# Kernel tuning notes

Hardware: AMD Instinct MI355X
Metric: run time of the kernel (lower is better)

## Reference

```python
import jax, jax.numpy as jnp
import numpy as np

K = 3        # kernel_size
DIL = 1      # dilation
PAD = 1      # padding (replicate)
RANKS = 3
STAGES = 9
C_OUT = 32


def setup_inputs() -> dict:
    key = jax.random.key(0)
    k1, k2, k3 = jax.random.split(key, 3)
    b, cin, H, W = 2, 3, 160, 160
    x = jax.random.normal(k1, (b, cin, H, W), dtype=jnp.float32)
    head_w = jax.random.normal(k2, (C_OUT, cin), dtype=jnp.float32) * (1.0 / np.sqrt(cin))
    tail_w = jax.random.normal(k3, (cin, C_OUT), dtype=jnp.float32) * (1.0 / np.sqrt(C_OUT))
    alphas = jnp.full((STAGES,), 0.01, dtype=jnp.float32)
    betas = jnp.full((STAGES,), 0.01, dtype=jnp.float32)
    return {"x": x, "head_w": head_w, "tail_w": tail_w, "alphas": alphas, "betas": betas}


def _unfold_like_torch(xp, H, W):
    # xp: [b, C, H+2p, W+2p] replicate-padded. Reproduce torch nn.Unfold output
    # layout [b, C*k*k, H*W] (channel-major, then ki, kj; L row-major over h,w).
    b, C = xp.shape[0], xp.shape[1]
    cols = [xp[:, :, i * DIL:i * DIL + H, j * DIL:j * DIL + W]
            for i in range(K) for j in range(K)]
    patches = jnp.stack(cols, axis=2)            # [b, C, k*k, H, W]
    return patches.reshape(b, C * K * K, H * W)  # torch unfold layout


def reference(x, head_w, tail_w, alphas, betas):
    b, cin, H, W = x.shape
    # head 1x1 conv (no bias) + relu
    xh = jax.nn.relu(jnp.einsum('bchw,oc->bohw', x, head_w))
    xp = jnp.pad(xh, ((0, 0), (0, 0), (PAD, PAD), (PAD, PAD)), mode='edge')
    Xu = _unfold_like_torch(xp, H, W)                 # [b, C*kk, H*W]
    # Faithful to torch: X = unfold.view(b, C, H, W, -1) (row-major reinterpret)
    X = Xu.reshape(b, C_OUT, H, W, K * K)
    U = jnp.repeat(X.mean(axis=-1, keepdims=True), RANKS, axis=-1)  # [b,C,H,W,r]
    V = jnp.repeat(X.mean(axis=1, keepdims=True), RANKS, axis=1)    # [b,r,H,W,kk]
    for i in range(STAGES):
        num_V = jnp.einsum('bchwr,bchwk->brhwk', U, X)
        UV = jnp.einsum('bchwr,brhwk->bchwk', U, V)
        den_V = jnp.einsum('bchwr,bchwk->brhwk', U, UV)
        V = V - betas[i] * (den_V - num_V)
        num_U = jnp.einsum('bchwk,brhwk->bchwr', X, V)
        UV = jnp.einsum('bchwr,brhwk->bchwk', U, V)
        den_U = jnp.einsum('bchwk,brhwk->bchwr', UV, V)
        U = U - alphas[i] * (den_U - num_U)
    center = (K // 2) * K + K // 2
    UVc = jnp.einsum('bchwr,brhwk->bchwk', U, V)[..., center]  # [b,C,H,W]
    out = jax.nn.relu(jnp.einsum('bchw,oc->bohw', UVc, tail_w))
    return out
```

## Files before the change

kernel.cpp:

```cpp
#include <hip/hip_runtime.h>
#include <hip/hip_bf16.h>

#define NB    2
#define HW    25600
#define WDIM  160
#define NSTG  9

template <int CTRL>
__device__ __forceinline__ float dpp_add(float v) {
    int moved = __builtin_amdgcn_update_dpp(0, __float_as_int(v), CTRL, 0xf, 0xf, true);
    return v + __int_as_float(moved);
}

__device__ __forceinline__ float reduce4(float v) {
    v = dpp_add<0xB1>(v);
    v = dpp_add<0x4E>(v);
    return v;
}

__global__ __launch_bounds__(256, 4) void fused_kernel(const float* __restrict__ x,
                                                       const float* __restrict__ head_w,
                                                       const float* __restrict__ tail_w,
                                                       const float* __restrict__ alphas,
                                                       const float* __restrict__ betas,
                                                       float* __restrict__ out) {
    int sub = threadIdx.x & 3;
    int pid = blockIdx.x * 64 + (threadIdx.x >> 2);
    int b   = blockIdx.x / 400;
    int s2  = pid - b * HW;
    int c0  = sub * 8;

    float al[NSTG], be[NSTG];
#pragma unroll
    for (int i = 0; i < NSTG; ++i) { al[i] = alphas[i]; be[i] = betas[i]; }

    const float* xb0 = x + b * 3 * HW;

    int g9  = s2 * 9;
    int kk0 = g9 / HW;
    int r0  = g9 - kk0 * HW;
    int h0  = r0 / WDIM;
    int w0  = r0 - h0 * WDIM;
    int ki0 = kk0 / 3;
    int dh0 = ki0 - 1,            dw0 = kk0 - ki0 * 3 - 1;
    int kk1 = kk0 + 1;
    int ki1 = kk1 / 3;
    int dh1 = ki1 - 1,            dw1 = kk1 - ki1 * 3 - 1;

    int p[9];
#pragma unroll
    for (int k2 = 0; k2 < 9; ++k2) {
        int r  = r0 + k2;
        int wn = w0 + k2;
        int cw = (wn >= WDIM);
        int w1 = cw ? wn - WDIM : wn;
        int h1 = h0 + cw;
        bool wr = (r >= HW);
        int h  = wr ? 0 : h1;
        int w  = wr ? r - HW : w1;
        int dh = wr ? dh1 : dh0;
        int dw = wr ? dw1 : dw0;
        int hh = min(max(h + dh, 0), 159);
        int ww = min(max(w + dw, 0), 159);
        p[k2]  = hh * WDIM + ww;
    }

    float xv0[9], xv1[9], xv2[9];
#pragma unroll
    for (int k2 = 0; k2 < 9; ++k2) xv0[k2] = xb0[p[k2]];
#pragma unroll
    for (int k2 = 0; k2 < 9; ++k2) xv1[k2] = xb0[HW + p[k2]];
#pragma unroll
    for (int k2 = 0; k2 < 9; ++k2) xv2[k2] = xb0[2 * HW + p[k2]];

    float X[9][8];
#pragma unroll
    for (int j = 0; j < 8; ++j) {
        float hwj0 = head_w[(c0 + j) * 3 + 0];
        float hwj1 = head_w[(c0 + j) * 3 + 1];
        float hwj2 = head_w[(c0 + j) * 3 + 2];
#pragma unroll
        for (int k2 = 0; k2 < 9; ++k2)
            X[k2][j] = fmaxf(hwj0 * xv0[k2] + hwj1 * xv1[k2] + hwj2 * xv2[k2], 0.f);
    }

    float u[8];
#pragma unroll
    for (int j = 0; j < 8; ++j) {
        float a = X[0][j];
#pragma unroll
        for (int k = 1; k < 9; ++k) a += X[k][j];
        u[j] = a * (1.f / 9.f);
    }
    float v[9];
#pragma unroll
    for (int k = 0; k < 9; ++k) {
        float pr = ((X[k][0] + X[k][1]) + (X[k][2] + X[k][3]))
                 + ((X[k][4] + X[k][5]) + (X[k][6] + X[k][7]));
        v[k] = reduce4(pr) * (1.f / 32.f);
    }

#pragma unroll
    for (int i = 0; i < NSTG; ++i) {
        float b3 = 3.f * be[i];
        float a3 = 3.f * al[i];
        float beta  = be[i];
        float alpha = al[i];
        float sp = ((u[0] * u[0] + u[1] * u[1]) + (u[2] * u[2] + u[3] * u[3]))
                 + ((u[4] * u[4] + u[5] * u[5]) + (u[6] * u[6] + u[7] * u[7]));
        float s  = reduce4(sp);
        float vs = 1.f - b3 * s;
#pragma unroll
        for (int k = 0; k < 9; ++k) {
            float qp = u[0] * X[k][0];
#pragma unroll
            for (int j = 1; j < 8; ++j) qp += u[j] * X[k][j];
            float q = reduce4(qp);
            v[k] = v[k] * vs + beta * q;
        }
        float t = (((v[0] * v[0] + v[1] * v[1]) + (v[2] * v[2] + v[3] * v[3]))
                +  ((v[4] * v[4] + v[5] * v[5]) + (v[6] * v[6] + v[7] * v[7])))
                +  v[8] * v[8];
        float us = 1.f - a3 * t;
#pragma unroll
        for (int j = 0; j < 8; ++j) {
            float m = X[0][j] * v[0];
#pragma unroll
            for (int k = 1; k < 9; ++k) m += X[k][j] * v[k];
            u[j] = u[j] * us + alpha * m;
        }
    }

    float v4 = v[4];
    float uvc[8];
#pragma unroll
    for (int j = 0; j < 8; ++j) uvc[j] = 3.f * u[j] * v4;
    float o[3];
#pragma unroll
    for (int oo = 0; oo < 3; ++oo) {
        const float* tw = tail_w + oo * 32 + c0;
        float pr = ((uvc[0] * tw[0] + uvc[1] * tw[1]) + (uvc[2] * tw[2] + uvc[3] * tw[3]))
                 + ((uvc[4] * tw[4] + uvc[5] * tw[5]) + (uvc[6] * tw[6] + uvc[7] * tw[7]));
        o[oo] = fmaxf(reduce4(pr), 0.f);
    }
    if (sub == 0) {
        float* op = out + b * 3 * HW + s2;
        op[0]      = o[0];
        op[HW]     = o[1];
        op[2 * HW] = o[2];
    }
}

extern "C" void kernel_launch(void* const* d_in, const int* in_sizes, int n_in,
                              void* d_out, int out_size, void* d_ws, size_t ws_size,
                              hipStream_t stream) {
    const float* x      = (const float*)d_in[0];
    const float* head_w = (const float*)d_in[1];
    const float* tail_w = (const float*)d_in[2];
    const float* alphas = (const float*)d_in[3];
    const float* betas  = (const float*)d_in[4];
    float*       out    = (float*)d_out;

    fused_kernel<<<dim3(NB * HW * 4 / 256), dim3(256), 0, stream>>>(
        x, head_w, tail_w, alphas, betas, out);
}
```

Baseline: 75.32 us.

## Represent U as X·a coefficients using 9x9 Gram matrix to skip per-stage reductions

Since U always lies in the span of X's columns (U = X·a), the kernel precomputes the 9x9 Gram matrix X^T X once (45 cross-lane reductions) and then runs all nine stages on 9-element coefficient vectors without touching X or doing DPP reductions. U is reconstructed from X and a only at the end. It also lowers launch bounds occupancy from 4 to 3 to allow more registers for the 45-entry Gram matrix. This trades per-stage wide dot products for a one-time Gram computation; the rearranged arithmetic can change floating-point rounding slightly.

```diff
diff --git a/kernel.cpp b/kernel.cpp
--- a/kernel.cpp
+++ b/kernel.cpp
@@ -18,7 +18,12 @@
     return v;
 }
 
-__global__ __launch_bounds__(256, 4) void fused_kernel(const float* __restrict__ x,
+__device__ __forceinline__ constexpr int hidx(int i, int j) {
+    return (i <= j) ? (9 * i - (i * (i - 1)) / 2 + (j - i))
+                    : (9 * j - (j * (j - 1)) / 2 + (i - j));
+}
+
+__global__ __launch_bounds__(256, 3) void fused_kernel(const float* __restrict__ x,
                                                        const float* __restrict__ head_w,
                                                        const float* __restrict__ tail_w,
                                                        const float* __restrict__ alphas,
@@ -84,14 +89,19 @@
             X[k2][j] = fmaxf(hwj0 * xv0[k2] + hwj1 * xv1[k2] + hwj2 * xv2[k2], 0.f);
     }
 
-    float u[8];
+    float Hm[45];
 #pragma unroll
-    for (int j = 0; j < 8; ++j) {
-        float a = X[0][j];
+    for (int i = 0; i < 9; ++i) {
 #pragma unroll
-        for (int k = 1; k < 9; ++k) a += X[k][j];
-        u[j] = a * (1.f / 9.f);
+        for (int j = i; j < 9; ++j) {
+            float hp = ((X[i][0] * X[j][0] + X[i][1] * X[j][1])
+                      + (X[i][2] * X[j][2] + X[i][3] * X[j][3]))
+                     + ((X[i][4] * X[j][4] + X[i][5] * X[j][5])
+                      + (X[i][6] * X[j][6] + X[i][7] * X[j][7]));
+            Hm[hidx(i, j)] = reduce4(hp);
+        }
     }
+
     float v[9];
 #pragma unroll
     for (int k = 0; k < 9; ++k) {
@@ -99,42 +109,52 @@
                  + ((X[k][4] + X[k][5]) + (X[k][6] + X[k][7]));
         v[k] = reduce4(pr) * (1.f / 32.f);
     }
+    float a[9];
+#pragma unroll
+    for (int k = 0; k < 9; ++k) a[k] = (1.f / 9.f);
 
 #pragma unroll
     for (int i = 0; i < NSTG; ++i) {
-        float b3 = 3.f * be[i];
-        float a3 = 3.f * al[i];
         float beta  = be[i];
         float alpha = al[i];
-        float sp = ((u[0] * u[0] + u[1] * u[1]) + (u[2] * u[2] + u[3] * u[3]))
-                 + ((u[4] * u[4] + u[5] * u[5]) + (u[6] * u[6] + u[7] * u[7]));
-        float s  = reduce4(sp);
-        float vs = 1.f - b3 * s;
+        float b3 = 3.f * beta;
+        float a3 = 3.f * alpha;
+        float c[9];
 #pragma unroll
-        for (int k = 0; k < 9; ++k) {
-            float qp = u[0] * X[k][0];
+        for (int r = 0; r < 9; ++r) {
+            float t0 = Hm[hidx(r, 0)] * a[0] + Hm[hidx(r, 1)] * a[1];
+            float t1 = Hm[hidx(r, 2)] * a[2] + Hm[hidx(r, 3)] * a[3];
+            float t2 = Hm[hidx(r, 4)] * a[4] + Hm[hidx(r, 5)] * a[5];
+            float t3 = Hm[hidx(r, 6)] * a[6] + Hm[hidx(r, 7)] * a[7];
+            c[r] = ((t0 + t1) + (t2 + t3)) + Hm[hidx(r, 8)] * a[8];
+        }
+        float S = (((a[0] * c[0] + a[1] * c[1]) + (a[2] * c[2] + a[3] * c[3]))
+                +  ((a[4] * c[4] + a[5] * c[5]) + (a[6] * c[6] + a[7] * c[7])))
+                +  a[8] * c[8];
+        float vs = 1.f - b3 * S;
 #pragma unroll
-            for (int j = 1; j < 8; ++j) qp += u[j] * X[k][j];
-            float q = reduce4(qp);
-            v[k] = v[k] * vs + beta * q;
-        }
-        float t = (((v[0] * v[0] + v[1] * v[1]) + (v[2] * v[2] + v[3] * v[3]))
+        for (int k = 0; k < 9; ++k)
+            v[k] = v[k] * vs + beta * c[k];
+        float T = (((v[0] * v[0] + v[1] * v[1]) + (v[2] * v[2] + v[3] * v[3]))
                 +  ((v[4] * v[4] + v[5] * v[5]) + (v[6] * v[6] + v[7] * v[7])))
                 +  v[8] * v[8];
-        float us = 1.f - a3 * t;
+        float us = 1.f - a3 * T;
 #pragma unroll
-        for (int j = 0; j < 8; ++j) {
-            float m = X[0][j] * v[0];
-#pragma unroll
-            for (int k = 1; k < 9; ++k) m += X[k][j] * v[k];
-            u[j] = u[j] * us + alpha * m;
-        }
+        for (int k = 0; k < 9; ++k)
+            a[k] = a[k] * us + alpha * v[k];
     }
 
     float v4 = v[4];
     float uvc[8];
 #pragma unroll
-    for (int j = 0; j < 8; ++j) uvc[j] = 3.f * u[j] * v4;
+    for (int j = 0; j < 8; ++j) {
+        float t0 = X[0][j] * a[0] + X[1][j] * a[1];
+        float t1 = X[2][j] * a[2] + X[3][j] * a[3];
+        float t2 = X[4][j] * a[4] + X[5][j] * a[5];
+        float t3 = X[6][j] * a[6] + X[7][j] * a[7];
+        float u  = ((t0 + t1) + (t2 + t3)) + X[8][j] * a[8];
+        uvc[j] = 3.f * u * v4;
+    }
     float o[3];
 #pragma unroll
     for (int oo = 0; oo < 3; ++oo) {
```

After: 81.33 us. 1.08x slower.
